# Optimization experiments

Measured on AMD Instinct MI355X. Metric: run time of the kernel, lower is better.

The kernel has to match this reference:

```python
import jax, jax.numpy as jnp
import numpy as np

N_HEAD, D_HEAD, D_MODEL = 16, 64, 1024
QLEN, MEMLEN, BSZ = 1024, 1024, 2
KLEN = QLEN + MEMLEN  # rlen == klen
LN_EPS = 1e-5
NEG = -1e30


def _rel_shift(x):
    # x: [qlen, rlen, bsz, n_head] -> Transformer-XL relative shift
    q, r, b, n = x.shape
    zp = jnp.zeros((q, 1, b, n), x.dtype)
    xp = jnp.concatenate([zp, x], axis=1).reshape(r + 1, q, b, n)
    return xp[1:].reshape(q, r, b, n)


def _layer_norm(x, gamma, beta):
    mu = jnp.mean(x, axis=-1, keepdims=True)
    var = jnp.mean((x - mu) ** 2, axis=-1, keepdims=True)
    return (x - mu) * jax.lax.rsqrt(var + LN_EPS) * gamma + beta


def setup_inputs() -> dict:
    key = jax.random.key(0)
    ks = jax.random.split(key, 8)
    w = jax.random.normal(ks[0], (QLEN, BSZ, D_MODEL), jnp.float32)
    r = jax.random.normal(ks[1], (KLEN, D_MODEL), jnp.float32)
    r_w_bias = jax.random.normal(ks[2], (N_HEAD, D_HEAD), jnp.float32) * 0.02
    r_r_bias = jax.random.normal(ks[3], (N_HEAD, D_HEAD), jnp.float32) * 0.02
    mems = jax.random.normal(ks[4], (MEMLEN, BSZ, D_MODEL), jnp.float32)
    W_qkv = jax.random.normal(ks[5], (D_MODEL, 3 * N_HEAD * D_HEAD), jnp.float32) * 0.02
    W_r = jax.random.normal(ks[6], (D_MODEL, N_HEAD * D_HEAD), jnp.float32) * 0.02
    W_o = jax.random.normal(ks[7], (N_HEAD * D_HEAD, D_MODEL), jnp.float32) * 0.02
    ln_gamma = jnp.ones((D_MODEL,), jnp.float32)
    ln_beta = jnp.zeros((D_MODEL,), jnp.float32)
    # causal mask with memory: key j visible to query i iff j <= i + MEMLEN (True = keep)
    attn_mask = jnp.arange(KLEN)[None, :] <= (jnp.arange(QLEN)[:, None] + MEMLEN)
    return {"w": w, "r": r, "r_w_bias": r_w_bias, "r_r_bias": r_r_bias,
            "mems": mems, "attn_mask": attn_mask, "W_qkv": W_qkv, "W_r": W_r,
            "W_o": W_o, "ln_gamma": ln_gamma, "ln_beta": ln_beta}


def reference(w, r, r_w_bias, r_r_bias, mems, attn_mask, W_qkv, W_r, W_o, ln_gamma, ln_beta):
    qlen, bsz = w.shape[0], w.shape[1]
    scale = 1.0 / (D_HEAD ** 0.5)
    cat = jnp.concatenate([mems, w], axis=0)            # [klen, b, d_model]
    klen = cat.shape[0]
    w_heads = cat @ W_qkv                                # [klen, b, 3*H*D]
    r_head_k = (r @ W_r).reshape(-1, N_HEAD, D_HEAD)     # [rlen, H, D]
    w_head_q, w_head_k, w_head_v = jnp.split(w_heads, 3, axis=-1)
    w_head_q = w_head_q[-qlen:].reshape(qlen, bsz, N_HEAD, D_HEAD)
    w_head_k = w_head_k.reshape(klen, bsz, N_HEAD, D_HEAD)
    w_head_v = w_head_v.reshape(klen, bsz, N_HEAD, D_HEAD)
    AC = jnp.einsum('ibnd,jbnd->ijbn', w_head_q + r_w_bias, w_head_k)
    BD = jnp.einsum('ibnd,jnd->ijbn', w_head_q + r_r_bias, r_head_k)
    BD = _rel_shift(BD)
    attn_score = (AC + BD) * scale                       # [q, k, b, n]
    attn_score = jnp.where(attn_mask[:, :, None, None], attn_score, NEG)
    attn_prob = jax.nn.softmax(attn_score, axis=1)
    attn_vec = jnp.einsum('ijbn,jbnd->ibnd', attn_prob, w_head_v)
    attn_vec = attn_vec.reshape(qlen, bsz, N_HEAD * D_HEAD)
    attn_out = attn_vec @ W_o                            # [q, b, d_model]
    return _layer_norm(w + attn_out, ln_gamma, ln_beta)
```

## Files before the change

### kernel.cpp

```cpp
#include <hip/hip_runtime.h>
#include <hip/hip_bf16.h>

#define NHEAD 16
#define DHEAD 64
#define DMODEL 1024
#define QLEN 1024
#define MEMLEN 1024
#define BSZ 2
#define KLEN 2048
#define LN_EPS 1e-5f

typedef __hip_bfloat16 bf16;
typedef __attribute__((ext_vector_type(8))) short short8;
typedef __attribute__((ext_vector_type(4))) float f32x4;

__device__ __forceinline__ float b2f(bf16 x) { return __bfloat162float(x); }
__device__ __forceinline__ bf16 f2b(float x) { return __float2bfloat16(x); }
__device__ __forceinline__ short f2bs(float f) {
    bf16 h = __float2bfloat16(f);
    return *reinterpret_cast<short*>(&h);
}
__device__ __forceinline__ float s2f(short s) {
    bf16 h = *reinterpret_cast<bf16*>(&s);
    return __bfloat162float(h);
}

#define MFMA16(a, b, c) __builtin_amdgcn_mfma_f32_16x16x32_bf16(a, b, c, 0, 0, 0)

#define AS1 __attribute__((address_space(1)))
#define AS3 __attribute__((address_space(3)))
__device__ __forceinline__ void gld16(const bf16* g, bf16* l) {
    __builtin_amdgcn_global_load_lds((const AS1 void*)(uintptr_t)g,
                                     (AS3 void*)(uint32_t)(uintptr_t)l, 16, 0, 0);
}

__global__ __launch_bounds__(256)
void prep(const float* __restrict__ mems, const float* __restrict__ w,
          const float* __restrict__ r, const float* __restrict__ Wqkv,
          const float* __restrict__ Wr, const float* __restrict__ Wo,
          bf16* __restrict__ Abf, bf16* __restrict__ rbf,
          bf16* __restrict__ Wqkvt, bf16* __restrict__ Wrt,
          bf16* __restrict__ Wot) {
    __shared__ bf16 T[64][65];
    const int id = blockIdx.x;
    const int t = threadIdx.x;
    if (id < 6144) {
        const float* src;
        bf16* dst;
        int off;
        if (id < 2048)      { src = mems; dst = Abf;                       off = id; }
        else if (id < 4096) { src = w;    dst = Abf + (size_t)2048 * 1024; off = id - 2048; }
        else                { src = r;    dst = rbf;                       off = id - 4096; }
        int i = off * 256 + t;
        const float4 v = reinterpret_cast<const float4*>(src)[i];
        bf16 o[4] = {f2b(v.x), f2b(v.y), f2b(v.z), f2b(v.w)};
        reinterpret_cast<ulong1*>(dst)[i] = *reinterpret_cast<ulong1*>(o);
        return;
    }
    int tid2 = id - 6144;
    const float* in;
    bf16* out;
    int N, tn, tile;
    if (tid2 < 768)       { in = Wqkv; out = Wqkvt; N = 3072; tn = 48; tile = tid2; }
    else if (tid2 < 1024) { in = Wr;   out = Wrt;   N = 1024; tn = 16; tile = tid2 - 768; }
    else                  { in = Wo;   out = Wot;   N = 1024; tn = 16; tile = tid2 - 1024; }
    const int K = 1024;
    const int n0 = (tile % tn) * 64, k0 = (tile / tn) * 64;
    #pragma unroll
    for (int e = 0; e < 16; e++) {
        int flat = e * 256 + t;
        int kl = flat >> 6, nl = flat & 63;
        T[kl][nl] = f2b(in[(size_t)(k0 + kl) * N + n0 + nl]);
    }
    __syncthreads();
    #pragma unroll
    for (int e = 0; e < 16; e++) {
        int flat = e * 256 + t;
        int nl = flat >> 6, kl = flat & 63;
        out[(size_t)(n0 + nl) * K + k0 + kl] = T[kl][nl];
    }
}

__global__ __launch_bounds__(256)
void gemm_mfma(const bf16* __restrict__ A, const bf16* __restrict__ Bt,
               const bf16* __restrict__ A2, const bf16* __restrict__ B2,
               int M, int N, int K, int mode,
               const float* __restrict__ rwb, const float* __restrict__ rrb,
               bf16* __restrict__ Qw, bf16* __restrict__ Qr,
               bf16* __restrict__ Kb, bf16* __restrict__ Vt,
               bf16* __restrict__ Cb, float* __restrict__ Cf) {
    const int bm = blockIdx.x * 128, bn = blockIdx.y * 128;
    int sub = 0;
    const bf16* Ap = A;
    const bf16* Bp = Bt;
    if (mode == 0 && bm < 2048 && bn < 1024) { sub = 1; Ap = A2; Bp = B2; }
    __shared__ bf16 As[128 * 32];
    __shared__ bf16 Bs[128 * 32];
    const int t = threadIdx.x;
    const int w = t >> 6, lane = t & 63, quad = lane >> 4, l16 = lane & 15;
    const int wm = (w >> 1) * 64, wn = (w & 1) * 64;
    const int lrow = lane >> 2, lcol = (lane & 3) * 8;

    f32x4 acc[4][4];
    #pragma unroll
    for (int mt = 0; mt < 4; mt++)
        #pragma unroll
        for (int nt = 0; nt < 4; nt++) acc[mt][nt] = (f32x4){0.f, 0.f, 0.f, 0.f};

    for (int k0 = 0; k0 < K; k0 += 32) {
        #pragma unroll
        for (int e = 0; e < 2; e++) {
            int ch = w + 4 * e;
            int row = ch * 16 + lrow;
            gld16(Ap + (size_t)(bm + row) * K + k0 + lcol, As + ch * 512);
            gld16(Bp + (size_t)(bn + row) * K + k0 + lcol, Bs + ch * 512);
        }
        __syncthreads();
        short8 af[4], bfr[4];
        #pragma unroll
        for (int mt = 0; mt < 4; mt++)
            af[mt] = *reinterpret_cast<short8*>(&As[(wm + 16 * mt + l16) * 32 + quad * 8]);
        #pragma unroll
        for (int nt = 0; nt < 4; nt++)
            bfr[nt] = *reinterpret_cast<short8*>(&Bs[(wn + 16 * nt + l16) * 32 + quad * 8]);
        #pragma unroll
        for (int mt = 0; mt < 4; mt++)
            #pragma unroll
            for (int nt = 0; nt < 4; nt++)
                acc[mt][nt] = MFMA16(af[mt], bfr[nt], acc[mt][nt]);
        __syncthreads();
    }

    #pragma unroll
    for (int mt = 0; mt < 4; mt++)
        #pragma unroll
        for (int nt = 0; nt < 4; nt++)
            #pragma unroll
            for (int r = 0; r < 4; r++) {
                int m = bm + wm + 16 * mt + quad * 4 + r;
                int c = bn + wn + 16 * nt + l16;
                float v = acc[mt][nt][r];
                if (sub) {
                    Cb[(size_t)m * 1024 + c] = f2b(v);
                } else if (mode == 0) {
                    int seg = c >> 10, cc = c & 1023;
                    if (seg == 0) {
                        if (m >= 2048) {
                            size_t o = (size_t)(m - 2048) * 1024 + cc;
                            Qw[o] = f2b(v + rwb[cc]);
                            Qr[o] = f2b(v + rrb[cc]);
                        }
                    } else if (seg == 1) {
                        Kb[(size_t)m * 1024 + cc] = f2b(v);
                    } else {
                        Vt[((size_t)cc * 2 + (m & 1)) * 2048 + (m >> 1)] = f2b(v);
                    }
                } else {
                    Cf[(size_t)m * N + c] = v;
                }
            }
}

__global__ __launch_bounds__(256, 3)
void attn_mfma(const bf16* __restrict__ Qw, const bf16* __restrict__ Qr,
               const bf16* __restrict__ Kb, const bf16* __restrict__ Vt,
               const bf16* __restrict__ Rk, bf16* __restrict__ AVbf) {
    const int id = blockIdx.x;
    const int xcd = id & 7, local = id >> 3;
    const int pair = xcd * 4 + (local & 3);
    const int i0 = local >> 2;
    const int b = pair & 1, n = pair >> 1;
    const int I0 = i0 * 64;

    const int tid = threadIdx.x;
    const int w = tid >> 6, lane = tid & 63;
    const int quad = lane >> 4, l16 = lane & 15;
    const int qbase = I0 + 16 * w;
    const int ln8 = lane >> 3;
    const int cs = (lane & 7) ^ (ln8 & 7);
    const int q0 = (quad ^ (l16 & 7)) * 8;
    const int q1 = q0 ^ 32;

    __shared__ bf16 Ks[64 * 64];
    __shared__ bf16 Vs[64 * 64];
    __shared__ bf16 Rs[128 * 64];
    __shared__ short WlB_s[4][16 * 80];
    __shared__ short Pb_s[4][16 * 72];
    short* WlB = WlB_s[w];
    short* Pb = Pb_s[w];

    short8 aqw[2], aqr[2];
    {
        const bf16* qp = Qw + ((size_t)(qbase + l16) * 2 + b) * 1024 + n * 64 + quad * 8;
        aqw[0] = *reinterpret_cast<const short8*>(qp);
        aqw[1] = *reinterpret_cast<const short8*>(qp + 32);
        const bf16* qp2 = Qr + ((size_t)(qbase + l16) * 2 + b) * 1024 + n * 64 + quad * 8;
        aqr[0] = *reinterpret_cast<const short8*>(qp2);
        aqr[1] = *reinterpret_cast<const short8*>(qp2 + 32);
    }

    f32x4 O[4];
    #pragma unroll
    for (int d = 0; d < 4; d++) O[d] = (f32x4){0.f, 0.f, 0.f, 0.f};
    float m_run = -1e30f;
    float pl[4] = {0.f, 0.f, 0.f, 0.f};

    const int T = i0 + 17;
    const int koff = b * 1024 + n * 64 + cs * 8;
    const size_t voff = (size_t)n * 262144 + b * 2048 + cs * 8;
    const int rcol = n * 64 + cs * 8;
    const int rbl = 48 - 16 * w;

    for (int tt = 0; tt < T; tt++) {
        const int J0 = tt * 64;
        const int RU0 = J0 - I0 + 960;

        #pragma unroll
        for (int e = 0; e < 2; e++) {
            int ch = w + 4 * e;
            int krow = J0 + ch * 8 + ln8;
            gld16(Kb + (size_t)krow * 2048 + koff, Ks + ch * 512);
            int dl = ch * 8 + ln8;
            gld16(Vt + (size_t)dl * 4096 + voff + J0, Vs + ch * 512);
        }
        #pragma unroll
        for (int e = 0; e < 4; e++) {
            int ch = w + 4 * e;
            int rrow = RU0 + ch * 8 + ln8;
            rrow = min(rrow, 2047);
            gld16(Rk + (size_t)rrow * 1024 + rcol, Rs + ch * 512);
        }
        __syncthreads();

        #pragma unroll
        for (int s = 0; s < 5; s++) {
            int rl = rbl + 16 * s + l16;
            short8 b0 = *reinterpret_cast<short8*>(&Rs[rl * 64 + q0]);
            short8 b1 = *reinterpret_cast<short8*>(&Rs[rl * 64 + q1]);
            f32x4 acc = (f32x4){0.f, 0.f, 0.f, 0.f};
            acc = MFMA16(aqr[0], b0, acc);
            acc = MFMA16(aqr[1], b1, acc);
            #pragma unroll
            for (int r = 0; r < 4; r++)
                WlB[(quad * 4 + r) * 80 + 16 * s + l16] = f2bs(acc[r]);
        }

        float sv[4][4];
        #pragma unroll
        for (int n16 = 0; n16 < 4; n16++) {
            int kr = 16 * n16 + l16;
            short8 k0 = *reinterpret_cast<short8*>(&Ks[kr * 64 + q0]);
            short8 k1 = *reinterpret_cast<short8*>(&Ks[kr * 64 + q1]);
            f32x4 acc = (f32x4){0.f, 0.f, 0.f, 0.f};
            acc = MFMA16(aqw[0], k0, acc);
            acc = MFMA16(aqw[1], k1, acc);
            #pragma unroll
            for (int r = 0; r < 4; r++) {
                int row = quad * 4 + r, col = 16 * n16 + l16;
                float s = (acc[r] + s2f(WlB[row * 80 + col - row + 15])) * 0.125f;
                if (J0 + col > qbase + row + MEMLEN) s = -1e30f;
                sv[n16][r] = s;
            }
        }

        float mx = sv[0][0];
        #pragma unroll
        for (int n16 = 0; n16 < 4; n16++)
            #pragma unroll
            for (int r = 0; r < 4; r++) mx = fmaxf(mx, sv[n16][r]);
        #pragma unroll
        for (int msk = 1; msk < 16; msk <<= 1) mx = fmaxf(mx, __shfl_xor(mx, msk));
        const float mn = fmaxf(m_run, mx);
        const float alpha = __expf(m_run - mn);
        m_run = mn;
        #pragma unroll
        for (int n16 = 0; n16 < 4; n16++)
            #pragma unroll
            for (int r = 0; r < 4; r++) sv[n16][r] = __expf(sv[n16][r] - mn);
        #pragma unroll
        for (int r = 0; r < 4; r++)
            pl[r] = pl[r] * alpha + (sv[0][r] + sv[1][r] + sv[2][r] + sv[3][r]);
        #pragma unroll
        for (int d = 0; d < 4; d++)
            #pragma unroll
            for (int r = 0; r < 4; r++) O[d][r] *= alpha;

        #pragma unroll
        for (int n16 = 0; n16 < 4; n16++)
            #pragma unroll
            for (int r = 0; r < 4; r++)
                Pb[(quad * 4 + r) * 72 + 16 * n16 + l16] = f2bs(sv[n16][r]);
        short8 ap0 = *reinterpret_cast<short8*>(&Pb[l16 * 72 + quad * 8]);
        short8 ap1 = *reinterpret_cast<short8*>(&Pb[l16 * 72 + 32 + quad * 8]);

        #pragma unroll
        for (int ds = 0; ds < 4; ds++) {
            int dr = 16 * ds + l16;
            short8 v0 = *reinterpret_cast<short8*>(&Vs[dr * 64 + q0]);
            short8 v1 = *reinterpret_cast<short8*>(&Vs[dr * 64 + q1]);
            O[ds] = MFMA16(ap0, v0, O[ds]);
            O[ds] = MFMA16(ap1, v1, O[ds]);
        }
        __syncthreads();
    }

    float lr[4];
    #pragma unroll
    for (int r = 0; r < 4; r++) {
        float s = pl[r];
        #pragma unroll
        for (int msk = 1; msk < 16; msk <<= 1) s += __shfl_xor(s, msk);
        lr[r] = s;
    }
    #pragma unroll
    for (int ds = 0; ds < 4; ds++)
        #pragma unroll
        for (int r = 0; r < 4; r++) {
            int q = qbase + quad * 4 + r;
            AVbf[((size_t)q * 2 + b) * 1024 + n * 64 + 16 * ds + l16] =
                f2b(O[ds][r] / lr[r]);
        }
}

__global__ __launch_bounds__(256)
void ln_res(const float* __restrict__ ao, const float* __restrict__ w,
            const float* __restrict__ gamma, const float* __restrict__ beta,
            float* __restrict__ out) {
    const int m = blockIdx.x;
    const int t = threadIdx.x;
    __shared__ float red[256];
    float x[4];
    #pragma unroll
    for (int e = 0; e < 4; e++) {
        int c = e * 256 + t;
        x[e] = ao[(size_t)m * DMODEL + c] + w[(size_t)m * DMODEL + c];
    }
    float s = x[0] + x[1] + x[2] + x[3];
    red[t] = s;
    __syncthreads();
    #pragma unroll
    for (int off = 128; off; off >>= 1) {
        if (t < off) red[t] += red[t + off];
        __syncthreads();
    }
    const float mu = red[0] * (1.f / 1024.f);
    __syncthreads();
    float s2 = 0.f;
    #pragma unroll
    for (int e = 0; e < 4; e++) { float dx = x[e] - mu; s2 += dx * dx; }
    red[t] = s2;
    __syncthreads();
    #pragma unroll
    for (int off = 128; off; off >>= 1) {
        if (t < off) red[t] += red[t + off];
        __syncthreads();
    }
    const float rstd = rsqrtf(red[0] * (1.f / 1024.f) + LN_EPS);
    #pragma unroll
    for (int e = 0; e < 4; e++) {
        int c = e * 256 + t;
        out[(size_t)m * DMODEL + c] = (x[e] - mu) * rstd * gamma[c] + beta[c];
    }
}

extern "C" void kernel_launch(void* const* d_in, const int* in_sizes, int n_in,
                              void* d_out, int out_size, void* d_ws, size_t ws_size,
                              hipStream_t stream) {
    const float* w        = (const float*)d_in[0];
    const float* r        = (const float*)d_in[1];
    const float* r_w_bias = (const float*)d_in[2];
    const float* r_r_bias = (const float*)d_in[3];
    const float* mems     = (const float*)d_in[4];
    const float* W_qkv    = (const float*)d_in[6];
    const float* W_r      = (const float*)d_in[7];
    const float* W_o      = (const float*)d_in[8];
    const float* gamma    = (const float*)d_in[9];
    const float* beta     = (const float*)d_in[10];
    float* out = (float*)d_out;

    bf16* Abf    = (bf16*)d_ws;
    bf16* Wqkvt  = Abf   + (size_t)4096 * 1024;
    bf16* Wrt    = Wqkvt + (size_t)3072 * 1024;
    bf16* Wot    = Wrt   + (size_t)1024 * 1024;
    bf16* rbf    = Wot   + (size_t)1024 * 1024;
    bf16* Qw     = rbf   + (size_t)2048 * 1024;
    bf16* Qr     = Qw    + (size_t)2048 * 1024;
    bf16* Kb     = Qr    + (size_t)2048 * 1024;
    bf16* Vt     = Kb    + (size_t)4096 * 1024;
    bf16* Rk     = Vt    + (size_t)2048 * 2048;
    bf16* AVbf   = Rk    + (size_t)2048 * 1024;
    float* attn_out = (float*)Abf;

    dim3 b256(256);
    prep<<<dim3(7424), b256, 0, stream>>>(mems, w, r, W_qkv, W_r, W_o,
                                          Abf, rbf, Wqkvt, Wrt, Wot);
    gemm_mfma<<<dim3(32, 24), b256, 0, stream>>>(
        Abf, Wqkvt, rbf, Wrt, 4096, 3072, 1024, 0, r_w_bias, r_r_bias,
        Qw, Qr, Kb, Vt, Rk, nullptr);
    attn_mfma<<<dim3(512), b256, 0, stream>>>(Qw, Qr, Kb, Vt, Rk, AVbf);
    gemm_mfma<<<dim3(16, 8), b256, 0, stream>>>(
        AVbf, Wot, nullptr, nullptr, 2048, 1024, 1024, 2, nullptr, nullptr,
        nullptr, nullptr, nullptr, nullptr, nullptr, attn_out);
    ln_res<<<dim3(QLEN * BSZ), b256, 0, stream>>>(attn_out, w, gamma, beta, out);
}
```

Measured before the change: 261.9 us.

## Double-buffer K/V and ring-buffer R tiles, balance causal blocks, lazy softmax rescale

Prefetches the next K/V tile and a future R tile into alternate shared-memory buffers while the current tile is computed, and reuses overlapping R tiles through a three-slot ring instead of reloading 128 rows each step. Block-to-work mapping is reordered so each XCD pairs short and long causal query tiles for load balance. The online-softmax rescale now happens only when the row max grows by more than a threshold, skipping the alpha multiply most of the time. Occupancy hint drops from 3 to 2 blocks per CU to leave room for the larger shared footprint. The single barrier per iteration with in-flight async loads into buffers that could still be read is a correctness risk.

```diff
diff --git a/kernel.cpp b/kernel.cpp
--- a/kernel.cpp
+++ b/kernel.cpp
@@ -161,14 +161,16 @@
             }
 }
 
-__global__ __launch_bounds__(256, 3)
+__global__ __launch_bounds__(256, 2)
 void attn_mfma(const bf16* __restrict__ Qw, const bf16* __restrict__ Qr,
                const bf16* __restrict__ Kb, const bf16* __restrict__ Vt,
                const bf16* __restrict__ Rk, bf16* __restrict__ AVbf) {
     const int id = blockIdx.x;
     const int xcd = id & 7, local = id >> 3;
-    const int pair = xcd * 4 + (local & 3);
-    const int i0 = local >> 2;
+    int i0, pidx;
+    if (local < 32) { i0 = local >> 1;              pidx = local & 1; }
+    else            { i0 = 15 - ((local - 32) >> 1); pidx = 2 + (local & 1); }
+    const int pair = xcd * 4 + pidx;
     const int b = pair & 1, n = pair >> 1;
     const int I0 = i0 * 64;
 
@@ -181,9 +183,9 @@
     const int q0 = (quad ^ (l16 & 7)) * 8;
     const int q1 = q0 ^ 32;
 
-    __shared__ bf16 Ks[64 * 64];
-    __shared__ bf16 Vs[64 * 64];
-    __shared__ bf16 Rs[128 * 64];
+    __shared__ bf16 Ks[2][64 * 64];
+    __shared__ bf16 Vs[2][64 * 64];
+    __shared__ bf16 Rs[3][64 * 64];
     __shared__ short WlB_s[4][16 * 80];
     __shared__ short Pb_s[4][16 * 72];
     short* WlB = WlB_s[w];
@@ -210,33 +212,50 @@
     const size_t voff = (size_t)n * 262144 + b * 2048 + cs * 8;
     const int rcol = n * 64 + cs * 8;
     const int rbl = 48 - 16 * w;
-
-    for (int tt = 0; tt < T; tt++) {
+    const int RB = 960 - I0;
+
+    auto stageKV = [&](int tt) {
         const int J0 = tt * 64;
-        const int RU0 = J0 - I0 + 960;
-
+        bf16* kd = Ks[tt & 1];
+        bf16* vd = Vs[tt & 1];
         #pragma unroll
         for (int e = 0; e < 2; e++) {
             int ch = w + 4 * e;
             int krow = J0 + ch * 8 + ln8;
-            gld16(Kb + (size_t)krow * 2048 + koff, Ks + ch * 512);
+            gld16(Kb + (size_t)krow * 2048 + koff, kd + ch * 512);
             int dl = ch * 8 + ln8;
-            gld16(Vt + (size_t)dl * 4096 + voff + J0, Vs + ch * 512);
-        }
-        #pragma unroll
-        for (int e = 0; e < 4; e++) {
+            gld16(Vt + (size_t)dl * 4096 + voff + J0, vd + ch * 512);
+        }
+    };
+    auto stageR = [&](int u) {
+        bf16* rd = Rs[u % 3];
+        #pragma unroll
+        for (int e = 0; e < 2; e++) {
             int ch = w + 4 * e;
-            int rrow = RU0 + ch * 8 + ln8;
-            rrow = min(rrow, 2047);
-            gld16(Rk + (size_t)rrow * 1024 + rcol, Rs + ch * 512);
-        }
-        __syncthreads();
+            int rrow = min(RB + u * 64 + ch * 8 + ln8, 2047);
+            gld16(Rk + (size_t)rrow * 1024 + rcol, rd + ch * 512);
+        }
+    };
+
+    stageKV(0); stageR(0); stageR(1);
+    __syncthreads();
+
+    for (int tt = 0; tt < T; tt++) {
+        if (tt + 1 < T) { stageKV(tt + 1); stageR(tt + 2); }
+
+        const bf16* K_ = Ks[tt & 1];
+        const bf16* V_ = Vs[tt & 1];
+        const bf16* R0 = Rs[tt % 3];
+        const bf16* R1 = Rs[(tt + 1) % 3];
+        const int J0 = tt * 64;
 
         #pragma unroll
         for (int s = 0; s < 5; s++) {
-            int rl = rbl + 16 * s + l16;
-            short8 b0 = *reinterpret_cast<short8*>(&Rs[rl * 64 + q0]);
-            short8 b1 = *reinterpret_cast<short8*>(&Rs[rl * 64 + q1]);
+            int rb2 = rbl + 16 * s;
+            const bf16* Rb = (rb2 & 64) ? R1 : R0;
+            int rh = (rb2 & 63) + l16;
+            short8 b0 = *reinterpret_cast<const short8*>(&Rb[rh * 64 + q0]);
+            short8 b1 = *reinterpret_cast<const short8*>(&Rb[rh * 64 + q1]);
             f32x4 acc = (f32x4){0.f, 0.f, 0.f, 0.f};
             acc = MFMA16(aqr[0], b0, acc);
             acc = MFMA16(aqr[1], b1, acc);
@@ -249,8 +268,8 @@
         #pragma unroll
         for (int n16 = 0; n16 < 4; n16++) {
             int kr = 16 * n16 + l16;
-            short8 k0 = *reinterpret_cast<short8*>(&Ks[kr * 64 + q0]);
-            short8 k1 = *reinterpret_cast<short8*>(&Ks[kr * 64 + q1]);
+            short8 k0 = *reinterpret_cast<const short8*>(&K_[kr * 64 + q0]);
+            short8 k1 = *reinterpret_cast<const short8*>(&K_[kr * 64 + q1]);
             f32x4 acc = (f32x4){0.f, 0.f, 0.f, 0.f};
             acc = MFMA16(aqw[0], k0, acc);
             acc = MFMA16(aqw[1], k1, acc);
@@ -270,20 +289,23 @@
             for (int r = 0; r < 4; r++) mx = fmaxf(mx, sv[n16][r]);
         #pragma unroll
         for (int msk = 1; msk < 16; msk <<= 1) mx = fmaxf(mx, __shfl_xor(mx, msk));
-        const float mn = fmaxf(m_run, mx);
-        const float alpha = __expf(m_run - mn);
-        m_run = mn;
+        if (mx > m_run + 8.f) {
+            const float alpha = __expf(m_run - mx);
+            m_run = mx;
+            #pragma unroll
+            for (int r = 0; r < 4; r++) pl[r] *= alpha;
+            #pragma unroll
+            for (int d = 0; d < 4; d++)
+                #pragma unroll
+                for (int r = 0; r < 4; r++) O[d][r] *= alpha;
+        }
         #pragma unroll
         for (int n16 = 0; n16 < 4; n16++)
             #pragma unroll
-            for (int r = 0; r < 4; r++) sv[n16][r] = __expf(sv[n16][r] - mn);
+            for (int r = 0; r < 4; r++) sv[n16][r] = __expf(sv[n16][r] - m_run);
         #pragma unroll
         for (int r = 0; r < 4; r++)
-            pl[r] = pl[r] * alpha + (sv[0][r] + sv[1][r] + sv[2][r] + sv[3][r]);
-        #pragma unroll
-        for (int d = 0; d < 4; d++)
-            #pragma unroll
-            for (int r = 0; r < 4; r++) O[d][r] *= alpha;
+            pl[r] += sv[0][r] + sv[1][r] + sv[2][r] + sv[3][r];
 
         #pragma unroll
         for (int n16 = 0; n16 < 4; n16++)
@@ -296,11 +318,12 @@
         #pragma unroll
         for (int ds = 0; ds < 4; ds++) {
             int dr = 16 * ds + l16;
-            short8 v0 = *reinterpret_cast<short8*>(&Vs[dr * 64 + q0]);
-            short8 v1 = *reinterpret_cast<short8*>(&Vs[dr * 64 + q1]);
+            short8 v0 = *reinterpret_cast<const short8*>(&V_[dr * 64 + q0]);
+            short8 v1 = *reinterpret_cast<const short8*>(&V_[dr * 64 + q1]);
             O[ds] = MFMA16(ap0, v0, O[ds]);
             O[ds] = MFMA16(ap1, v1, O[ds]);
         }
+
         __syncthreads();
     }
 
```

Result: no change. 259.0 us (-1.1%).
